# Kernel optimization log

Measured on AMD Instinct MI355X. Metric: run time of the kernel, lower is better.

The kernel has to match this reference:

```python
import jax, jax.numpy as jnp
import numpy as np

B, C, H, W = 4, 64, 64, 64  # x shape; mask is (B,1,8H,8W)


def _conv(x, w, pad=0):
    return jax.lax.conv_general_dilated(
        x, w, (1, 1), [(pad, pad), (pad, pad)],
        dimension_numbers=('NCHW', 'OIHW', 'NCHW'))


def _inorm(x, eps=1e-5):  # InstanceNorm2d, affine=False, biased var (torch default)
    mu = x.mean(axis=(2, 3), keepdims=True)
    var = x.var(axis=(2, 3), keepdims=True)
    return (x - mu) * jax.lax.rsqrt(var + eps)


def _forward(x, mask, kconv_w1, kconv_w2, fs_w1, fs_w2, fs_b2, fs_fuse_w):
    b, c, h, w = x.shape
    n = h * w
    # MaxPool2d(8,8) then binarize
    m = jax.lax.reduce_window(mask, -jnp.inf, jax.lax.max,
                              (1, 1, 8, 8), (1, 1, 8, 8), 'VALID')
    m = (m > 0).astype(x.dtype)
    back = 1.0 - m
    # ResidualBlock K_conv (shared for K and Q paths in original code)
    y = jax.nn.relu(_inorm(_conv(x, kconv_w1, pad=1)))
    y = _inorm(_conv(y, kconv_w2, pad=1))
    kx = jax.nn.relu(y + x)
    # L2-normalized K/Q over channel dim
    K = (kx * back).reshape(b, c, n)
    K = K / (jnp.linalg.norm(K, axis=1, keepdims=True) + 1e-8)
    Q = (kx * m).reshape(b, c, n)
    Q = Q / (jnp.linalg.norm(Q, axis=1, keepdims=True) + 1e-8)
    V = (x * back).reshape(b, c, n)
    # cosine-similarity score map, temperature 20
    score = jnp.einsum('bcq,bck->bqk', Q, K) * 20.0  # (b, n_q, n_k)
    qm = m.reshape(b, 1, n)      # query mask (foreground)
    km = back.reshape(b, 1, n)   # key mask (background)
    NEG = -1000000.0
    validx = score + (1.0 - km) * NEG + (1.0 - qm.transpose(0, 2, 1)) * NEG
    att = jax.nn.softmax(validx, axis=-1) * (qm.transpose(0, 2, 1) * km)
    # att_fore[b,c,q] = sum_k V[b,c,k] * att[b,q,k]
    att_fore = jnp.einsum('bck,bqk->bcq', V, att).reshape(b, c, h, w)
    # Fusion_score
    feat1 = _conv(jnp.concatenate([x * m, att_fore * m], axis=1), fs_w1)
    s = jax.nn.sigmoid(_conv(feat1, fs_w2) + fs_b2[None, :, None, None])
    fused = _conv(jnp.concatenate([x * m, att_fore * m * (1.0 - s)], axis=1), fs_fuse_w)
    fs_out = fused * m + x * (1.0 - m)
    out = fs_out * m + x * (1.0 - m)
    # visualization attention mask
    visatt = att.sum(axis=1).reshape(b, 1, h, w)
    attmask = jnp.repeat(jnp.repeat(visatt, 8, axis=2), 8, axis=3)  # nearest upsample x8
    attmask = attmask / attmask.max()
    return out, attmask


def setup_inputs() -> dict:
    key = jax.random.key(0)
    ks = jax.random.split(key, 8)

    def wgt(k, shape, fan_in):
        return jax.random.normal(k, shape, jnp.float32) / np.sqrt(fan_in)

    x = jax.random.normal(ks[0], (B, C, H, W), jnp.float32)
    # sparse foreground mask so maxpool(8x8)>0 yields a mixed fg/bg mask
    mask = (jax.random.uniform(ks[1], (B, 1, H * 8, W * 8)) < 0.01).astype(jnp.float32)
    return dict(
        x=x, mask=mask,
        kconv_w1=wgt(ks[2], (C, C, 3, 3), C * 9),
        kconv_w2=wgt(ks[3], (C, C, 3, 3), C * 9),
        fs_w1=wgt(ks[4], (C, 2 * C, 1, 1), 2 * C),
        fs_w2=wgt(ks[5], (C, C, 1, 1), C),
        fs_b2=jnp.zeros((C,), jnp.float32),
        fs_fuse_w=wgt(ks[6], (C, 2 * C, 1, 1), 2 * C),
    )


def reference(x, mask, kconv_w1, kconv_w2, fs_w1, fs_w2, fs_b2, fs_fuse_w):
    return _forward(x, mask, kconv_w1, kconv_w2, fs_w1, fs_w2, fs_b2, fs_fuse_w)
```

## Files before the change

### kernel.cpp

```cpp
#include <hip/hip_runtime.h>
#include <hip/hip_bf16.h>

typedef __hip_bfloat16 bf16;
typedef __attribute__((ext_vector_type(8))) short short8;
typedef __attribute__((ext_vector_type(4))) float f32x4;
typedef __attribute__((ext_vector_type(16))) float f32x16;

#define BB 4
#define CC 64
#define NN 4096
#define MH 512
#define MW 512
#define LS 72

#define WB_AFC  ((size_t)0)
#define WB_DEN  ((size_t)4194304)
#define WB_VIS  ((size_t)4259840)
#define WB_QIX  ((size_t)4325376)
#define WB_KIX  ((size_t)4390912)
#define WB_MFL  ((size_t)4456448)
#define WB_CNT  ((size_t)4472832)
#define WB_STAT ((size_t)4472896)
#define WB_WT1  ((size_t)4476992)
#define WB_WT2  ((size_t)4550720)
#define WB_WFB  ((size_t)4624448)
#define WB_XT   ((size_t)8388608)
#define WB_KXT  ((size_t)10485760)
#define WB_E    ((size_t)16777216)
#define EB_ELEM ((size_t)8388608)

__device__ __forceinline__ float b2f(bf16 v) { return __bfloat162float(v); }
__device__ __forceinline__ float us2f(unsigned short u) { return __uint_as_float(((unsigned)u) << 16); }
__device__ __forceinline__ unsigned short f2bu(float f) {
  bf16 h = __float2bfloat16(f);
  return *(unsigned short*)&h;
}

__global__ __launch_bounds__(256) void k_pre(const float* __restrict__ x,
                                             const float* __restrict__ mask,
                                             const float* __restrict__ w1,
                                             const float* __restrict__ w2,
                                             const float* __restrict__ fw1,
                                             const float* __restrict__ fw2,
                                             const float* __restrict__ fwf,
                                             float* __restrict__ outp,
                                             unsigned short* __restrict__ xt,
                                             unsigned char* __restrict__ mfl,
                                             float* __restrict__ vis,
                                             float* __restrict__ gstat,
                                             unsigned int* __restrict__ vmaxb,
                                             unsigned short* __restrict__ wT1,
                                             unsigned short* __restrict__ wT2,
                                             unsigned short* __restrict__ wfb) {
  __shared__ float lx[64][65];
  int t = threadIdx.x;
  if (blockIdx.x < 256) {
    int b = blockIdx.x >> 6, p0 = (blockIdx.x & 63) * 64;
    const float* xb = x + (size_t)b * CC * NN + p0;
    float* ob = outp + (size_t)b * CC * NN + p0;
    for (int idx = t; idx < 4096; idx += 256) {
      int c = idx >> 6, j = idx & 63;
      float v = xb[c * NN + j];
      lx[j][c] = v;
      ob[c * NN + j] = v;
    }
    __syncthreads();
    unsigned short* xo = xt + ((size_t)b * NN + p0) * 64;
    for (int idx = t; idx < 2048; idx += 256) {
      int j = idx >> 5, c2 = (idx & 31) * 2;
      ushort2 w2v;
      w2v.x = f2bu(lx[j][c2]);
      w2v.y = f2bu(lx[j][c2 + 1]);
      *(ushort2*)&xo[j * 64 + c2] = w2v;
    }
  } else {
    int g = (blockIdx.x - 256) * 256 + t;
    int o = g >> 2, sub = g & 3;
    int b = o >> 12, p = o & 4095;
    int py = p >> 6, px = p & 63;
    const float* mb = mask + (size_t)b * MH * MW + (py * 8 + sub * 2) * MW + px * 8;
    float mx = 0.f;
    #pragma unroll
    for (int dy = 0; dy < 2; ++dy) {
      const float4* r4 = (const float4*)(mb + dy * MW);
      float4 a = r4[0], c = r4[1];
      mx = fmaxf(mx, fmaxf(fmaxf(a.x, a.y), fmaxf(a.z, a.w)));
      mx = fmaxf(mx, fmaxf(fmaxf(c.x, c.y), fmaxf(c.z, c.w)));
    }
    mx = fmaxf(mx, __shfl_xor(mx, 1));
    mx = fmaxf(mx, __shfl_xor(mx, 2));
    if (sub == 0) {
      mfl[o] = (mx > 0.f) ? 1 : 0;
      vis[o] = 0.f;
    }
    if (g < 1024) gstat[g] = 0.f;
    if (g == 0) vmaxb[0] = 0u;
    if (g < 36864) {
      int tap = g >> 12;
      int rem = g & 4095;
      int co = rem >> 6, ci = rem & 63;
      int src = (co * 64 + ci) * 9 + tap;
      wT1[g] = f2bu(w1[src]);
      wT2[g] = f2bu(w2[src]);
    } else if (g < 57344) {
      int j2 = g - 36864;
      if (j2 < 8192)       wfb[j2] = f2bu(fw1[j2]);
      else if (j2 < 12288) wfb[j2] = f2bu(fw2[j2 - 8192]);
      else                 wfb[j2] = f2bu(fwf[j2 - 12288]);
    }
  }
}

__global__ __launch_bounds__(256) void k_compact(const unsigned char* __restrict__ mfl,
                                                 int* __restrict__ qidx, int* __restrict__ kidx,
                                                 int* __restrict__ nq, int* __restrict__ nk) {
  int b = blockIdx.x;
  __shared__ unsigned char lm[4096];
  int t = threadIdx.x;
  *(uint4*)&lm[t * 16] = *(const uint4*)&mfl[b * NN + t * 16];
  __syncthreads();
  if (t >= 64) return;
  int lane = t;
  int qb = 0, kb = 0;
  #pragma unroll
  for (int it = 0; it < 64; ++it) {
    int p = it * 64 + lane;
    bool f = lm[p] != 0;
    unsigned long long bal = __ballot(f);
    int before = __popcll(bal & ((1ULL << lane) - 1ULL));
    if (f)  qidx[b * NN + qb + before] = p;
    if (!f) kidx[b * NN + kb + (lane - before)] = p;
    int cnt = __popcll(bal);
    qb += cnt; kb += 64 - cnt;
  }
  if (lane == 0) { nq[b] = qb; nk[b] = kb; }
}

template <bool NORM_IN>
__global__ __launch_bounds__(256) void k_convm(const unsigned short* __restrict__ src,
                                               const unsigned short* __restrict__ wT,
                                               const float* __restrict__ insum,
                                               const float* __restrict__ insq,
                                               unsigned short* __restrict__ dst,
                                               float* __restrict__ gsum,
                                               float* __restrict__ gsq) {
  int b = blockIdx.y;
  int r = blockIdx.x;
  __shared__ unsigned short bx[198 * LS];
  __shared__ float nmean[64], ninv[64];
  int t = threadIdx.x;
  if (NORM_IN) {
    if (t < 64) {
      float m = insum[b * 64 + t] * (1.f / NN);
      float v = fmaxf(insq[b * 64 + t] * (1.f / NN) - m * m, 0.f);
      nmean[t] = m; ninv[t] = rsqrtf(v + 1e-5f);
    }
    __syncthreads();
  }
  const unsigned short* sb = src + (size_t)b * NN * 64;
  for (int idx = t; idx < 198 * 8; idx += 256) {
    int row = idx >> 3, c8 = (idx & 7) * 8;
    int dy = row / 66;
    int cx = row - dy * 66 - 1;
    int rr = r + dy - 1;
    uint4 v = make_uint4(0u, 0u, 0u, 0u);
    if ((unsigned)rr < 64u && (unsigned)cx < 64u) {
      v = *(const uint4*)(sb + ((size_t)(rr * 64 + cx)) * 64 + c8);
      if (NORM_IN) {
        unsigned short* e = (unsigned short*)&v;
        #pragma unroll
        for (int j = 0; j < 8; ++j)
          e[j] = f2bu(fmaxf((us2f(e[j]) - nmean[c8 + j]) * ninv[c8 + j], 0.f));
      }
    }
    *(uint4*)&bx[row * LS + c8] = v;
  }
  __syncthreads();
  int lane = t & 63;
  int quad = lane >> 4, col = lane & 15;
  int qw = (t >> 6) * 16;
  f32x4 acc[4] = {{0.f,0.f,0.f,0.f},{0.f,0.f,0.f,0.f},{0.f,0.f,0.f,0.f},{0.f,0.f,0.f,0.f}};
  #pragma unroll
  for (int tap = 0; tap < 9; ++tap) {
    int dy = tap / 3, dx = tap - dy * 3 - 1;
    const unsigned short* wrow = wT + ((size_t)tap * 64 + qw + col) * 64;
    short8 a0 = *(const short8*)(wrow + quad * 8);
    short8 a1 = *(const short8*)(wrow + 32 + quad * 8);
    int rbase = dy * 66 + dx + 1;
    #pragma unroll
    for (int nt = 0; nt < 4; ++nt) {
      int row = rbase + nt * 16 + col;
      short8 b0 = *(const short8*)&bx[row * LS + quad * 8];
      short8 b1 = *(const short8*)&bx[row * LS + 32 + quad * 8];
      acc[nt] = __builtin_amdgcn_mfma_f32_16x16x32_bf16(a0, b0, acc[nt], 0, 0, 0);
      acc[nt] = __builtin_amdgcn_mfma_f32_16x16x32_bf16(a1, b1, acc[nt], 0, 0, 0);
    }
  }
  #pragma unroll
  for (int rr = 0; rr < 4; ++rr) {
    float s1 = acc[0][rr] + acc[1][rr] + acc[2][rr] + acc[3][rr];
    float s2 = acc[0][rr]*acc[0][rr] + acc[1][rr]*acc[1][rr]
             + acc[2][rr]*acc[2][rr] + acc[3][rr]*acc[3][rr];
    s1 += __shfl_xor(s1, 1); s2 += __shfl_xor(s2, 1);
    s1 += __shfl_xor(s1, 2); s2 += __shfl_xor(s2, 2);
    s1 += __shfl_xor(s1, 4); s2 += __shfl_xor(s2, 4);
    s1 += __shfl_xor(s1, 8); s2 += __shfl_xor(s2, 8);
    if (col == 0) {
      int co = qw + quad * 4 + rr;
      atomicAdd(&gsum[b * 64 + co], s1);
      atomicAdd(&gsq[b * 64 + co], s2);
    }
  }
  __syncthreads();
  #pragma unroll
  for (int nt = 0; nt < 4; ++nt)
    #pragma unroll
    for (int rr = 0; rr < 4; ++rr)
      bx[(nt * 16 + col) * LS + qw + quad * 4 + rr] = f2bu(acc[nt][rr]);
  __syncthreads();
  unsigned short* db = dst + ((size_t)b * NN + r * 64) * 64;
  for (int idx = t; idx < 512; idx += 256) {
    int px = idx >> 3, c8 = (idx & 7) * 8;
    *(uint4*)(db + (size_t)px * 64 + c8) = *(const uint4*)&bx[px * LS + c8];
  }
}

__global__ __launch_bounds__(256) void k_knorm(unsigned short* __restrict__ kxt,
                                               const unsigned short* __restrict__ xt,
                                               const float* __restrict__ gsum,
                                               const float* __restrict__ gsq,
                                               float* __restrict__ afc,
                                               float* __restrict__ den) {
  int b = blockIdx.x >> 6;
  int p0 = (blockIdx.x & 63) * 64;
  __shared__ float m2[64], i2[64];
  int t = threadIdx.x;
  if (t < 64) {
    float m = gsum[b * 64 + t] * (1.f / NN);
    float v = fmaxf(gsq[b * 64 + t] * (1.f / NN) - m * m, 0.f);
    m2[t] = m; i2[t] = rsqrtf(v + 1e-5f);
  }
  size_t gid = (size_t)blockIdx.x * 256 + t;
  float4 z4 = make_float4(0.f, 0.f, 0.f, 0.f);
  float4* az = (float4*)afc;
  #pragma unroll
  for (int j = 0; j < 4; ++j) az[gid + (size_t)j * 65536] = z4;
  if (gid < 16384) den[gid] = 0.f;
  __syncthreads();
  int px = t >> 2, c0 = (t & 3) * 16;
  size_t base = ((size_t)b * NN + p0 + px) * 64 + c0;
  unsigned short kv[16], xv[16];
  *(uint4*)&kv[0] = *(const uint4*)(kxt + base);
  *(uint4*)&kv[8] = *(const uint4*)(kxt + base + 8);
  *(uint4*)&xv[0] = *(const uint4*)(xt + base);
  *(uint4*)&xv[8] = *(const uint4*)(xt + base + 8);
  float v[16]; float ss = 0.f;
  #pragma unroll
  for (int j = 0; j < 16; ++j) {
    float f = fmaxf((us2f(kv[j]) - m2[c0 + j]) * i2[c0 + j] + us2f(xv[j]), 0.f);
    v[j] = f; ss += f * f;
  }
  ss += __shfl_xor(ss, 1);
  ss += __shfl_xor(ss, 2);
  float inv = 1.f / (sqrtf(ss) + 1e-8f);
  #pragma unroll
  for (int j = 0; j < 16; ++j) kv[j] = f2bu(v[j] * inv);
  *(uint4*)(kxt + base) = *(const uint4*)&kv[0];
  *(uint4*)(kxt + base + 8) = *(const uint4*)&kv[8];
}

__global__ __launch_bounds__(256) void k_att1(const unsigned short* __restrict__ khat,
                                              const unsigned short* __restrict__ xt,
                                              const int* __restrict__ qidx, const int* __restrict__ kidx,
                                              const int* __restrict__ nqv, const int* __restrict__ nkv,
                                              float* __restrict__ afc, float* __restrict__ den,
                                              unsigned short* __restrict__ eg) {
  int b = blockIdx.y;
  int nqb = nqv[b], nkb = nkv[b];
  int q0 = (blockIdx.x >> 3) * 64;
  int part = blockIdx.x & 7;
  if (q0 >= nqb) return;
  int kbeg = (part * nkb) >> 3;
  int kend = ((part + 1) * nkb) >> 3;
  int NKP = (nkb + 63) & ~63;
  __shared__ unsigned short lk [64 * LS];
  __shared__ unsigned short lvT[64 * LS];
  __shared__ unsigned short le [64 * LS];
  int t = threadIdx.x;
  int wave = t >> 6, lane = t & 63;
  int l31 = lane & 31, lhi = lane >> 5;
  int qh = wave >> 1, kh = wave & 1;
  const int* qix = qidx + b * NN;
  const int* kix = kidx + b * NN;
  const unsigned short* khb = khat + (size_t)b * NN * 64;
  const unsigned short* xtb = xt + (size_t)b * NN * 64;
  unsigned short* egb = eg + (size_t)b * EB_ELEM;
  int qq_a = q0 + qh * 32 + l31;
  int qp_a = (qq_a < nqb) ? qix[qq_a] : qix[0];
  short8 aq[4];
  #pragma unroll
  for (int ks = 0; ks < 4; ++ks)
    aq[ks] = *(const short8*)(khb + (size_t)qp_a * 64 + ks * 16 + lhi * 8);
  f32x16 pv, dsum;
  #pragma unroll
  for (int i = 0; i < 16; ++i) { pv[i] = 0.f; dsum[i] = 0.f; }
  int kp2 = t >> 3, vc8 = (t & 7) * 8, vcc = (t & 7);
  for (int j0 = kbeg; j0 < kend; j0 += 64) {
    __syncthreads();
    for (int idx = t; idx < 512; idx += 256) {
      int k = idx >> 3, c8 = (idx & 7) * 8;
      uint4 v = make_uint4(0u, 0u, 0u, 0u);
      if (j0 + k < kend) v = *(const uint4*)(khb + (size_t)kix[j0 + k] * 64 + c8);
      *(uint4*)&lk[k * LS + c8] = v;
    }
    {
      uint4 v0 = make_uint4(0u, 0u, 0u, 0u);
      uint4 v1 = make_uint4(0u, 0u, 0u, 0u);
      int ka = j0 + 2 * kp2, kb2 = ka + 1;
      if (ka  < kend) v0 = *(const uint4*)(xtb + (size_t)kix[ka]  * 64 + vc8);
      if (kb2 < kend) v1 = *(const uint4*)(xtb + (size_t)kix[kb2] * 64 + vc8);
      const unsigned short* e0 = (const unsigned short*)&v0;
      const unsigned short* e1 = (const unsigned short*)&v1;
      int pbase = kp2 & 3, prun = kp2 >> 2;
      int pp = pbase + ((prun ^ vcc) << 2);
      #pragma unroll
      for (int jj = 0; jj < 8; ++jj) {
        int c = vc8 + jj;
        unsigned int w2 = (unsigned)e0[jj] | ((unsigned)e1[jj] << 16);
        *(unsigned int*)&lvT[c * LS + pp * 2] = w2;
      }
    }
    __syncthreads();
    f32x16 s;
    #pragma unroll
    for (int i = 0; i < 16; ++i) s[i] = 0.f;
    #pragma unroll
    for (int ks = 0; ks < 4; ++ks) {
      short8 bk = *(const short8*)&lk[(kh * 32 + l31) * LS + ks * 16 + lhi * 8];
      s = __builtin_amdgcn_mfma_f32_32x32x16_bf16(aq[ks], bk, s, 0, 0, 0);
    }
    bool kval = (j0 + kh * 32 + l31) < kend;
    unsigned short* egc = egb + (size_t)(j0 + kh * 32 + l31);
    #pragma unroll
    for (int reg = 0; reg < 16; ++reg) {
      float e = kval ? __expf(20.f * s[reg]) : 0.f;
      dsum[reg] += e;
      int row = (reg & 3) + 8 * (reg >> 2) + 4 * lhi;
      unsigned short eh = f2bu(e);
      le[(qh * 32 + row) * LS + kh * 32 + l31] = eh;
      int qq = q0 + qh * 32 + row;
      if (kval && qq < nqb) egc[(size_t)qq * NKP] = eh;
    }
    __syncthreads();
    int c = kh * 32 + l31;
    int c37 = (c >> 3) & 7;
    #pragma unroll
    for (int ks = 0; ks < 4; ++ks) {
      short8 a  = *(const short8*)&le[(qh * 32 + l31) * LS + ks * 16 + lhi * 8];
      int run = ks * 2 + lhi;
      short8 bv = *(const short8*)&lvT[c * LS + ((run ^ c37) << 3)];
      pv = __builtin_amdgcn_mfma_f32_32x32x16_bf16(a, bv, pv, 0, 0, 0);
    }
  }
  #pragma unroll
  for (int reg = 0; reg < 16; ++reg) {
    float v = dsum[reg];
    v += __shfl_xor(v, 1); v += __shfl_xor(v, 2); v += __shfl_xor(v, 4);
    v += __shfl_xor(v, 8); v += __shfl_xor(v, 16);
    int row = (reg & 3) + 8 * (reg >> 2) + 4 * lhi;
    int qq = q0 + qh * 32 + row;
    if (l31 == 0 && qq < nqb) atomicAdd(&den[b * NN + qq], v);
  }
  #pragma unroll
  for (int reg = 0; reg < 16; ++reg) {
    int row = (reg & 3) + 8 * (reg >> 2) + 4 * lhi;
    int qq = q0 + qh * 32 + row;
    if (qq < nqb) atomicAdd(&afc[((size_t)b * NN + qq) * 64 + kh * 32 + l31], pv[reg]);
  }
}

__global__ __launch_bounds__(256) void k_vis(const unsigned short* __restrict__ eg,
                                             const float* __restrict__ den,
                                             const int* __restrict__ kidx,
                                             const int* __restrict__ nqv, const int* __restrict__ nkv,
                                             float* __restrict__ vis) {
  int b = blockIdx.z;
  int nqb = nqv[b], nkb = nkv[b];
  int k0 = blockIdx.x * 256;
  if (k0 >= nkb) return;
  int NKP = (nkb + 63) & ~63;
  int qpart = blockIdx.y;
  int qbeg = (qpart * nqb) >> 3;
  int qend = ((qpart + 1) * nqb) >> 3;
  __shared__ float wd[256];
  int t = threadIdx.x;
  int k = k0 + t;
  const unsigned short* eb = eg + (size_t)b * EB_ELEM;
  float acc = 0.f;
  for (int qc = qbeg; qc < qend; qc += 256) {
    __syncthreads();
    int qq = qc + t;
    float d = (qq < qend) ? den[b * NN + qq] : 0.f;
    wd[t] = (d > 0.f) ? 1.f / d : 0.f;
    __syncthreads();
    int lim = min(256, qend - qc);
    if (k < nkb) {
      const unsigned short* ep = eb + (size_t)qc * NKP + k;
      int j = 0;
      for (; j + 8 <= lim; j += 8) {
        #pragma unroll
        for (int u = 0; u < 8; ++u)
          acc += us2f(ep[(size_t)(j + u) * NKP]) * wd[j + u];
      }
      for (; j < lim; ++j)
        acc += us2f(ep[(size_t)j * NKP]) * wd[j];
    }
  }
  if (k < nkb) atomicAdd(&vis[b * NN + kidx[b * NN + k]], acc);
}

#define FS 136
__global__ __launch_bounds__(256) void k_fusionm(const unsigned short* __restrict__ xt,
                                                 const float* __restrict__ afc,
                                                 const float* __restrict__ den,
                                                 const int* __restrict__ qidx, const int* __restrict__ nqv,
                                                 const unsigned short* __restrict__ wall,
                                                 const float* __restrict__ b2,
                                                 float* __restrict__ outp) {
  int b = blockIdx.y;
  int nqb = nqv[b];
  int q0 = blockIdx.x * 64;
  if (q0 >= nqb) return;
  __shared__ unsigned short pxa[64 * FS];
  __shared__ unsigned short f1s[64 * LS];
  __shared__ int qpl[64];
  int t = threadIdx.x;
  int lane = t & 63;
  int quad = lane >> 4, col = lane & 15;
  int cb = (t >> 6) * 16;
  const int* qix = qidx + b * NN;
  const unsigned short* xtb = xt + (size_t)b * NN * 64;
  const unsigned short* w1b = wall;
  const unsigned short* w2b = wall + 8192;
  const unsigned short* wfb = wall + 12288;
  short8 a1[4], a2[2], af[4];
  #pragma unroll
  for (int kt = 0; kt < 4; ++kt) {
    a1[kt] = *(const short8*)&w1b[(cb + col) * 128 + kt * 32 + quad * 8];
    af[kt] = *(const short8*)&wfb[(cb + col) * 128 + kt * 32 + quad * 8];
  }
  #pragma unroll
  for (int kt = 0; kt < 2; ++kt)
    a2[kt] = *(const short8*)&w2b[(cb + col) * 64 + kt * 32 + quad * 8];
  float b2v[4];
  #pragma unroll
  for (int r = 0; r < 4; ++r) b2v[r] = b2[cb + quad * 4 + r];
  if (t < 64) qpl[t] = (q0 + t < nqb) ? qix[q0 + t] : -1;
  for (int idx = t; idx < 512; idx += 256) {
    int q = idx >> 3, c8 = (idx & 7) * 8;
    int qq = q0 + q;
    uint4 pv = make_uint4(0u, 0u, 0u, 0u);
    unsigned short pa8[8] = {0, 0, 0, 0, 0, 0, 0, 0};
    if (qq < nqb) {
      int qp = qix[qq];
      pv = *(const uint4*)(xtb + (size_t)qp * 64 + c8);
      float d = den[b * NN + qq];
      float invd = (d > 0.f) ? 1.f / d : 0.f;
      const float* ap = afc + ((size_t)b * NN + qq) * 64 + c8;
      #pragma unroll
      for (int j = 0; j < 8; ++j) pa8[j] = f2bu(ap[j] * invd);
    }
    *(uint4*)&pxa[q * FS + c8] = pv;
    *(uint4*)&pxa[q * FS + 64 + c8] = *(const uint4*)&pa8[0];
  }
  __syncthreads();
  #pragma unroll
  for (int qt = 0; qt < 4; ++qt) {
    f32x4 acc = {0.f, 0.f, 0.f, 0.f};
    #pragma unroll
    for (int kt = 0; kt < 4; ++kt) {
      short8 bfrag = *(const short8*)&pxa[(qt * 16 + col) * FS + kt * 32 + quad * 8];
      acc = __builtin_amdgcn_mfma_f32_16x16x32_bf16(a1[kt], bfrag, acc, 0, 0, 0);
    }
    #pragma unroll
    for (int r = 0; r < 4; ++r)
      f1s[(qt * 16 + col) * LS + cb + quad * 4 + r] = f2bu(acc[r]);
  }
  __syncthreads();
  #pragma unroll
  for (int qt = 0; qt < 4; ++qt) {
    f32x4 acc = {0.f, 0.f, 0.f, 0.f};
    #pragma unroll
    for (int kt = 0; kt < 2; ++kt) {
      short8 bfrag = *(const short8*)&f1s[(qt * 16 + col) * LS + kt * 32 + quad * 8];
      acc = __builtin_amdgcn_mfma_f32_16x16x32_bf16(a2[kt], bfrag, acc, 0, 0, 0);
    }
    #pragma unroll
    for (int r = 0; r < 4; ++r) {
      float sg = 1.f / (1.f + __expf(-(acc[r] + b2v[r])));
      int addr = (qt * 16 + col) * FS + 64 + cb + quad * 4 + r;
      pxa[addr] = f2bu(us2f(pxa[addr]) * (1.f - sg));
    }
  }
  __syncthreads();
  #pragma unroll
  for (int qt = 0; qt < 4; ++qt) {
    f32x4 acc = {0.f, 0.f, 0.f, 0.f};
    #pragma unroll
    for (int kt = 0; kt < 4; ++kt) {
      short8 bfrag = *(const short8*)&pxa[(qt * 16 + col) * FS + kt * 32 + quad * 8];
      acc = __builtin_amdgcn_mfma_f32_16x16x32_bf16(af[kt], bfrag, acc, 0, 0, 0);
    }
    int qp = qpl[qt * 16 + col];
    if (qp >= 0) {
      #pragma unroll
      for (int r = 0; r < 4; ++r)
        outp[((size_t)b * CC + cb + quad * 4 + r) * NN + qp] = acc[r];
    }
  }
}

__global__ __launch_bounds__(256) void k_vmax(const float* __restrict__ vis, unsigned int* __restrict__ vmaxb) {
  int i = blockIdx.x * 256 + threadIdx.x;
  float v = vis[i];
  #pragma unroll
  for (int off = 32; off > 0; off >>= 1) v = fmaxf(v, __shfl_down(v, off));
  if ((threadIdx.x & 63) == 0) atomicMax(vmaxb, __float_as_uint(v));
}

__global__ __launch_bounds__(256) void k_upsample(const float* __restrict__ vis,
                                                  const unsigned int* __restrict__ vmaxb,
                                                  float* __restrict__ out2) {
  int i = blockIdx.x * 256 + threadIdx.x;
  int b = i >> 18;
  int rem = i & 262143;
  int y = rem >> 9, x = rem & 511;
  float vm = __uint_as_float(vmaxb[0]);
  if (!(vm > 0.f)) vm = 1.f;
  out2[i] = vis[b * NN + (y >> 3) * 64 + (x >> 3)] / vm;
}

extern "C" void kernel_launch(void* const* d_in, const int* in_sizes, int n_in,
                              void* d_out, int out_size, void* d_ws, size_t ws_size,
                              hipStream_t stream) {
  const float* x    = (const float*)d_in[0];
  const float* mask = (const float*)d_in[1];
  const float* w1   = (const float*)d_in[2];
  const float* w2c  = (const float*)d_in[3];
  const float* fsw1 = (const float*)d_in[4];
  const float* fsw2 = (const float*)d_in[5];
  const float* fsb2 = (const float*)d_in[6];
  const float* fswf = (const float*)d_in[7];
  float* out = (float*)d_out;
  char* wsb = (char*)d_ws;

  float* afc = (float*)(wsb + WB_AFC);
  float* den = (float*)(wsb + WB_DEN);
  float* vis = (float*)(wsb + WB_VIS);
  int* qidx  = (int*)(wsb + WB_QIX);
  int* kidx  = (int*)(wsb + WB_KIX);
  unsigned char* mfl = (unsigned char*)(wsb + WB_MFL);
  int* nq = (int*)(wsb + WB_CNT);
  int* nk = nq + 4;
  unsigned int* vmaxb = (unsigned int*)(nq + 8);
  float* gstat = (float*)(wsb + WB_STAT);
  float* gsum1 = gstat;
  float* gsq1  = gstat + 256;
  float* gsum2 = gstat + 512;
  float* gsq2  = gstat + 768;
  unsigned short* wT1 = (unsigned short*)(wsb + WB_WT1);
  unsigned short* wT2 = (unsigned short*)(wsb + WB_WT2);
  unsigned short* wall = (unsigned short*)(wsb + WB_WFB);
  unsigned short* y1t = (unsigned short*)(wsb + WB_AFC);
  unsigned short* xt  = (unsigned short*)(wsb + WB_XT);
  unsigned short* kxt = (unsigned short*)(wsb + WB_KXT);
  unsigned short* khat = kxt;
  unsigned short* eg  = (unsigned short*)(wsb + WB_E);

  k_pre<<<512, 256, 0, stream>>>(x, mask, w1, w2c, fsw1, fsw2, fswf,
                                 out, xt, mfl, vis, gstat, vmaxb, wT1, wT2, wall);
  k_compact<<<4, 256, 0, stream>>>(mfl, qidx, kidx, nq, nk);
  k_convm<false><<<dim3(64, BB), 256, 0, stream>>>(xt, wT1, nullptr, nullptr, y1t, gsum1, gsq1);
  k_convm<true><<<dim3(64, BB), 256, 0, stream>>>(y1t, wT2, gsum1, gsq1, kxt, gsum2, gsq2);
  k_knorm<<<256, 256, 0, stream>>>(kxt, xt, gsum2, gsq2, afc, den);
  k_att1<<<dim3(512, BB), 256, 0, stream>>>(khat, xt, qidx, kidx, nq, nk, afc, den, eg);
  k_vis<<<dim3(16, 8, BB), 256, 0, stream>>>(eg, den, kidx, nq, nk, vis);
  k_fusionm<<<dim3(64, BB), 256, 0, stream>>>(xt, afc, den, qidx, nq, wall, fsb2, out);
  k_vmax<<<64, 256, 0, stream>>>(vis, vmaxb);
  k_upsample<<<4096, 256, 0, stream>>>(vis, vmaxb, out + 1048576);
}
```

Baseline: 191.2 us.

## Interleave key tiles across parts, prefetch gathers, and vectorize score stores

The k_att1 kernel now gives each of the 8 parts 64-wide key tiles in round-robin order instead of one contiguous key range. It stages the key indices in shared memory and issues the next tile's K and V gather loads into registers before the current tile's MFMA work, so the loads overlap the compute. The scattered per-element bf16 stores of the exp scores are replaced by coalesced 16-byte stores copied out of the shared score tile. This costs extra registers and a 2KB shared index buffer, and it assumes the tile-aligned padding of the score buffer.

```diff
diff --git a/kernel.cpp b/kernel.cpp
--- a/kernel.cpp
+++ b/kernel.cpp
@@ -280,12 +280,14 @@
   int q0 = (blockIdx.x >> 3) * 64;
   int part = blockIdx.x & 7;
   if (q0 >= nqb) return;
-  int kbeg = (part * nkb) >> 3;
-  int kend = ((part + 1) * nkb) >> 3;
+  int ntiles = (nkb + 63) >> 6;
+  int nt_blk = (part < ntiles) ? ((ntiles - part + 7) >> 3) : 0;
+  if (nt_blk == 0) return;
   int NKP = (nkb + 63) & ~63;
   __shared__ unsigned short lk [64 * LS];
   __shared__ unsigned short lvT[64 * LS];
   __shared__ unsigned short le [64 * LS];
+  __shared__ int lidxa[512];
   int t = threadIdx.x;
   int wave = t >> 6, lane = t & 63;
   int l31 = lane & 31, lhi = lane >> 5;
@@ -301,36 +303,44 @@
   #pragma unroll
   for (int ks = 0; ks < 4; ++ks)
     aq[ks] = *(const short8*)(khb + (size_t)qp_a * 64 + ks * 16 + lhi * 8);
+  for (int idx = t; idx < nt_blk * 64; idx += 256) {
+    int it = idx >> 6, k = idx & 63;
+    lidxa[idx] = kix[(part + it * 8) * 64 + k];
+  }
+  __syncthreads();
+  int klo = t >> 3, c8 = (t & 7) * 8, vcc = t & 7;
+  uint4 g0, g1, g2, g3;
+  auto issue_gather = [&](int it) {
+    int j0 = (part + it * 8) * 64;
+    const int* lp = lidxa + it * 64;
+    uint4 z = make_uint4(0u, 0u, 0u, 0u);
+    g0 = (j0 + klo      < nkb) ? *(const uint4*)(khb + (size_t)lp[klo] * 64 + c8) : z;
+    g1 = (j0 + klo + 32 < nkb) ? *(const uint4*)(khb + (size_t)lp[klo + 32] * 64 + c8) : z;
+    g2 = (j0 + 2 * klo     < nkb) ? *(const uint4*)(xtb + (size_t)lp[2 * klo] * 64 + c8) : z;
+    g3 = (j0 + 2 * klo + 1 < nkb) ? *(const uint4*)(xtb + (size_t)lp[2 * klo + 1] * 64 + c8) : z;
+  };
+  issue_gather(0);
   f32x16 pv, dsum;
   #pragma unroll
   for (int i = 0; i < 16; ++i) { pv[i] = 0.f; dsum[i] = 0.f; }
-  int kp2 = t >> 3, vc8 = (t & 7) * 8, vcc = (t & 7);
-  for (int j0 = kbeg; j0 < kend; j0 += 64) {
+  for (int it = 0; it < nt_blk; ++it) {
+    int j0 = (part + it * 8) * 64;
     __syncthreads();
-    for (int idx = t; idx < 512; idx += 256) {
-      int k = idx >> 3, c8 = (idx & 7) * 8;
-      uint4 v = make_uint4(0u, 0u, 0u, 0u);
-      if (j0 + k < kend) v = *(const uint4*)(khb + (size_t)kix[j0 + k] * 64 + c8);
-      *(uint4*)&lk[k * LS + c8] = v;
-    }
+    *(uint4*)&lk[klo * LS + c8] = g0;
+    *(uint4*)&lk[(klo + 32) * LS + c8] = g1;
     {
-      uint4 v0 = make_uint4(0u, 0u, 0u, 0u);
-      uint4 v1 = make_uint4(0u, 0u, 0u, 0u);
-      int ka = j0 + 2 * kp2, kb2 = ka + 1;
-      if (ka  < kend) v0 = *(const uint4*)(xtb + (size_t)kix[ka]  * 64 + vc8);
-      if (kb2 < kend) v1 = *(const uint4*)(xtb + (size_t)kix[kb2] * 64 + vc8);
-      const unsigned short* e0 = (const unsigned short*)&v0;
-      const unsigned short* e1 = (const unsigned short*)&v1;
-      int pbase = kp2 & 3, prun = kp2 >> 2;
+      const unsigned short* e0 = (const unsigned short*)&g2;
+      const unsigned short* e1 = (const unsigned short*)&g3;
+      int pbase = klo & 3, prun = klo >> 2;
       int pp = pbase + ((prun ^ vcc) << 2);
       #pragma unroll
       for (int jj = 0; jj < 8; ++jj) {
-        int c = vc8 + jj;
         unsigned int w2 = (unsigned)e0[jj] | ((unsigned)e1[jj] << 16);
-        *(unsigned int*)&lvT[c * LS + pp * 2] = w2;
+        *(unsigned int*)&lvT[(c8 + jj) * LS + pp * 2] = w2;
       }
     }
     __syncthreads();
+    if (it + 1 < nt_blk) issue_gather(it + 1);
     f32x16 s;
     #pragma unroll
     for (int i = 0; i < 16; ++i) s[i] = 0.f;
@@ -339,19 +349,20 @@
       short8 bk = *(const short8*)&lk[(kh * 32 + l31) * LS + ks * 16 + lhi * 8];
       s = __builtin_amdgcn_mfma_f32_32x32x16_bf16(aq[ks], bk, s, 0, 0, 0);
     }
-    bool kval = (j0 + kh * 32 + l31) < kend;
-    unsigned short* egc = egb + (size_t)(j0 + kh * 32 + l31);
+    bool kval = (j0 + kh * 32 + l31) < nkb;
     #pragma unroll
     for (int reg = 0; reg < 16; ++reg) {
       float e = kval ? __expf(20.f * s[reg]) : 0.f;
       dsum[reg] += e;
       int row = (reg & 3) + 8 * (reg >> 2) + 4 * lhi;
-      unsigned short eh = f2bu(e);
-      le[(qh * 32 + row) * LS + kh * 32 + l31] = eh;
-      int qq = q0 + qh * 32 + row;
-      if (kval && qq < nqb) egc[(size_t)qq * NKP] = eh;
+      le[(qh * 32 + row) * LS + kh * 32 + l31] = f2bu(e);
     }
     __syncthreads();
+    for (int idx = t; idx < 512; idx += 256) {
+      int q = idx >> 3, cc8 = (idx & 7) * 8;
+      if (q0 + q < nqb)
+        *(uint4*)(egb + (size_t)(q0 + q) * NKP + j0 + cc8) = *(const uint4*)&le[q * LS + cc8];
+    }
     int c = kh * 32 + l31;
     int c37 = (c >> 3) & 7;
     #pragma unroll
```

After: 184.6 us. 1.04x faster.
